# Performance work log

Hardware: AMD Instinct MI355X
Metric: run time of the kernel (lower is better)

The kernel has to match this reference:

```python
import jax, jax.numpy as jnp
import numpy as np

B, C2, H, W = 4, 1024, 64, 64  # features have 2*input_dim channels
CH = C2 // 2                   # 512 = input_dim
HID = CH // 4                  # 128 = hidden_channels


def setup_inputs() -> dict:
    key = jax.random.key(0)
    ks = jax.random.split(key, 6)
    left = jax.random.normal(ks[0], (B, C2, H, W), dtype=jnp.float32)
    right = jax.random.normal(ks[1], (B, C2, H, W), dtype=jnp.float32)
    # 1x1 conv params (weight [out,in], bias [out]) for query/reference projections
    Wq = jax.random.normal(ks[2], (HID, CH), dtype=jnp.float32) * 0.02
    bq = jax.random.normal(ks[3], (HID,), dtype=jnp.float32) * 0.02
    Wk = jax.random.normal(ks[4], (HID, CH), dtype=jnp.float32) * 0.02
    bk = jax.random.normal(ks[5], (HID,), dtype=jnp.float32) * 0.02
    return {"left_features": left, "right_features": right, "Wq": Wq, "bq": bq, "Wk": Wk, "bk": bk}


def _co_attention(qf, rf, Wq, bq, Wk, bk):
    # 1x1 convs == per-pixel channel matmuls
    Q = jnp.einsum('bchw,oc->bohw', qf, Wq) + bq[None, :, None, None]   # [B,HID,H,W]
    K = jnp.einsum('bchw,oc->bohw', rf, Wk) + bk[None, :, None, None]   # [B,HID,H,W]
    b, c, h, w = Q.shape
    Kf = K.reshape(b, c, h * w)                                          # [B,HID,P]
    V = rf.reshape(rf.shape[0], rf.shape[1], h * w)                      # [B,CH,P]
    # attention_map: einsum('bcij,bckl->bijkl') then flatten (kl) == contract channels
    attn = jnp.einsum('bcij,bcp->bijp', Q, Kf)                           # [B,H,W,P]
    attn = jax.nn.softmax(attn, axis=3)
    return jnp.einsum('bijp,bcp->bcij', attn, V)                         # [B,CH,H,W]


def _homo(qf, rf):
    weights = jax.nn.softmax(qf - rf, axis=1)  # softmax over channels
    return rf * weights


def _get_both_differences(q, r, Wq, bq, Wk, bk):
    c = q.shape[1] // 2
    q_orig, q_trans = q[:, :c], q[:, c:]
    r_orig = r[:, :c]
    cross = _co_attention(q_orig, r_orig, Wq, bq, Wk, bk)
    reduce = _homo(q_orig, q_trans)
    return jnp.concatenate([q_orig, cross + reduce], axis=1)


def reference(left_features, right_features, Wq, bq, Wk, bk):
    left_out = _get_both_differences(left_features, right_features, Wq, bq, Wk, bk)
    right_out = _get_both_differences(right_features, left_features, Wq, bq, Wk, bk)
    return (left_out, right_out)
```

## Files before the change

### kernel.cpp

```cpp
#include <hip/hip_runtime.h>
#include <hip/hip_bf16.h>

#define NB 4
#define LOG2E 1.4426950408889634f

typedef unsigned short u16;
typedef __attribute__((ext_vector_type(8))) short bf16x8;
typedef __attribute__((ext_vector_type(4))) float f32x4;

static __device__ __forceinline__ float bf2f(u16 u) {
    union { float f; unsigned v; } x; x.v = ((unsigned)u) << 16; return x.f;
}
static __device__ __forceinline__ u16 f2bf(float f) {
    unsigned v = __builtin_bit_cast(unsigned, f);
    return (u16)((v + 0x7FFFu + ((v >> 16) & 1u)) >> 16);
}
static __device__ __forceinline__ void gload_lds16(const u16* g, u16* l) {
    __builtin_amdgcn_global_load_lds(
        (const __attribute__((address_space(1))) unsigned*)(const void*)g,
        (__attribute__((address_space(3))) unsigned*)(void*)l, 16, 0, 0);
}

__global__ void k_wcvt(const float* __restrict__ Wq, const float* __restrict__ Wk,
                       u16* __restrict__ Wbq, u16* __restrict__ Wbk) {
    int i = blockIdx.x * 1024 + threadIdx.x;
    Wbq[i] = f2bf(Wq[i]);
    Wbk[i] = f2bf(Wk[i]);
}

__global__ void k_cvt(const float* __restrict__ L, const float* __restrict__ R,
                      u16* __restrict__ Lb, u16* __restrict__ Rb, float* __restrict__ out) {
    int i = blockIdx.x * 256 + threadIdx.x;
    int pq = i & 1023;
    int c = (i >> 10) & 511;
    int b = (i >> 19) & 3;
    int side = i >> 21;
    const float* src = (side ? R : L) + ((long)(b * 1024 + c) << 12) + (pq << 2);
    float4 v = *reinterpret_cast<const float4*>(src);
    ushort4 u;
    u.x = f2bf(v.x); u.y = f2bf(v.y); u.z = f2bf(v.z); u.w = f2bf(v.w);
    *reinterpret_cast<ushort4*>((side ? Rb : Lb) + ((long)(b * 512 + c) << 12) + (pq << 2)) = u;
    *reinterpret_cast<float4*>(out + ((long)(side * 4 + b) * 1024 + c) * 4096 + (pq << 2)) = v;
}

__global__ __launch_bounds__(256) void k_proj(
        const u16* __restrict__ Lb, const u16* __restrict__ Rb,
        const u16* __restrict__ Wbq, const u16* __restrict__ Wbk,
        const float* __restrict__ bq, const float* __restrict__ bk,
        u16* __restrict__ QL, u16* __restrict__ KL,
        u16* __restrict__ QR, u16* __restrict__ KR) {
    __shared__ u16 XT[2][64 * 40];
    int pj = blockIdx.x & 15, pt = blockIdx.x >> 4;
    int ty = pj >> 2, b = pj & 3;
    const u16* src; const u16* Wb; const float* bias; u16* dst;
    if (ty == 0)      { src = Lb; Wb = Wbq; bias = bq; dst = QL; }
    else if (ty == 1) { src = Rb; Wb = Wbk; bias = bk; dst = KL; }
    else if (ty == 2) { src = Rb; Wb = Wbq; bias = bq; dst = QR; }
    else              { src = Lb; Wb = Wbk; bias = bk; dst = KR; }
    const u16* X = src + (long)b * 512 * 4096 + pt * 64;
    int tid = threadIdx.x;
    int wv = __builtin_amdgcn_readfirstlane(tid >> 6);
    int lane = tid & 63, g = lane >> 4, li = lane & 15;

    f32x4 acc[8];
#pragma unroll
    for (int ob = 0; ob < 8; ob++)
#pragma unroll
        for (int r = 0; r < 4; r++) acc[ob][r] = bias[ob * 16 + g * 4 + r];

    int c_r = tid >> 3, j = tid & 7;
    bf16x8 gx = *reinterpret_cast<const bf16x8*>(X + (long)c_r * 4096 + j * 8);
#pragma unroll
    for (int k = 0; k < 8; k++) XT[0][(j * 8 + k) * 40 + c_r] = (u16)gx[k];
    __syncthreads();

    for (int cc = 0; cc < 16; cc++) {
        int buf = cc & 1;
        bf16x8 gn;
        if (cc < 15)
            gn = *reinterpret_cast<const bf16x8*>(X + (long)(cc * 32 + 32 + c_r) * 4096 + j * 8);
        bf16x8 xb = *reinterpret_cast<const bf16x8*>(&XT[buf][(wv * 16 + li) * 40 + g * 8]);
#pragma unroll
        for (int ob = 0; ob < 8; ob++) {
            bf16x8 aw = *reinterpret_cast<const bf16x8*>(Wb + (long)(ob * 16 + li) * 512 + cc * 32 + g * 8);
            acc[ob] = __builtin_amdgcn_mfma_f32_16x16x32_bf16(aw, xb, acc[ob], 0, 0, 0);
        }
        if (cc < 15) {
#pragma unroll
            for (int k = 0; k < 8; k++) XT[buf ^ 1][(j * 8 + k) * 40 + c_r] = (u16)gn[k];
        }
        __syncthreads();
    }
    u16* d = dst + ((long)b * 4096 + pt * 64 + wv * 16 + li) * 128;
#pragma unroll
    for (int ob = 0; ob < 8; ob++) {
        uint2 w;
        w.x = (unsigned)f2bf(acc[ob][0]) | ((unsigned)f2bf(acc[ob][1]) << 16);
        w.y = (unsigned)f2bf(acc[ob][2]) | ((unsigned)f2bf(acc[ob][3]) << 16);
        *reinterpret_cast<uint2*>(d + ob * 16 + g * 4) = w;
    }
}

__global__ __launch_bounds__(512, 4) void k_qk(
        const u16* __restrict__ QL, const u16* __restrict__ KL,
        const u16* __restrict__ QR, const u16* __restrict__ KR,
        u16* __restrict__ P, float* __restrict__ sums,
        int bd0, int bdMask, int bdShift) {
    __shared__ u16 Kl[2][8192];
    __shared__ u16 Ps[4096];
    __shared__ float sred[4][2][16];
    int bdl = (int)blockIdx.x & bdMask;
    int rest = (int)blockIdx.x >> bdShift;
    int qtile = rest & 63;
    int ph0 = rest >> 6;
    int bd = bd0 + bdl, dir = bd & 1, b = bd >> 1;
    const u16* Qt = (dir ? QR : QL) + (size_t)b * 4096 * 128;
    const u16* Kt = (dir ? KR : KL) + (size_t)b * 4096 * 128;
    u16* Pbd = P + ((size_t)bdl << 24);
    int q0 = qtile * 64;
    int tid = threadIdx.x;
    int wv = __builtin_amdgcn_readfirstlane(tid >> 6);
    int lane = tid & 63, g = lane >> 4, li = lane & 15;
    int qt = wv >> 1, phw = wv & 1;

#define STAGE_K(BUF, PT)                                                                   \
    {                                                                                      \
        _Pragma("unroll") for (int r0 = 0; r0 < 2; r0++) {                                 \
            int o = r0 * 8192 + tid * 16;                                                  \
            int row = o >> 8, w = o & 255;                                                 \
            int sw = (w ^ ((row & 7) << 4)) >> 1;                                          \
            gload_lds16(Kt + (((size_t)((PT) * 64 + row)) << 7) + sw,                      \
                        &Kl[BUF][r0 * 4096 + wv * 512]);                                   \
        }                                                                                  \
    }

    bf16x8 qf[4];
#pragma unroll
    for (int hc = 0; hc < 4; hc++)
        qf[hc] = *reinterpret_cast<const bf16x8*>(
            Qt + (size_t)(q0 + qt * 16 + li) * 128 + hc * 32 + g * 8);
    float psum = 0.f;
    STAGE_K(0, ph0 * 32)

    for (int tt = 0; tt < 32; tt++) {
        int pt = ph0 * 32 + tt;
        if (tt == 0) asm volatile("s_waitcnt vmcnt(0) lgkmcnt(0)\n\ts_barrier" ::: "memory");
        else         asm volatile("s_waitcnt vmcnt(1) lgkmcnt(0)\n\ts_barrier" ::: "memory");
        if (tt < 31) STAGE_K((tt + 1) & 1, pt + 1)
        int buf = tt & 1;
        f32x4 sv[2];
        sv[0] = (f32x4){0.f, 0.f, 0.f, 0.f};
        sv[1] = (f32x4){0.f, 0.f, 0.f, 0.f};
        __builtin_amdgcn_s_setprio(1);
#pragma unroll
        for (int ps = 0; ps < 2; ps++) {
            int row = phw * 32 + ps * 16 + li;
            unsigned rb = (unsigned)row * 256;
            unsigned sz = (unsigned)((row & 7) << 4);
#pragma unroll
            for (int hc = 0; hc < 4; hc++) {
                bf16x8 kf = *reinterpret_cast<const bf16x8*>(
                    (char*)Kl[buf] + rb + (((unsigned)(hc * 64 + g * 16)) ^ sz));
                sv[ps] = __builtin_amdgcn_mfma_f32_16x16x32_bf16(kf, qf[hc], sv[ps], 0, 0, 0);
            }
        }
        __builtin_amdgcn_s_setprio(0);
        int qrow = qt * 16 + li;
        unsigned qsz = (unsigned)((qrow & 7) << 4);
#pragma unroll
        for (int ps = 0; ps < 2; ps++) {
            float e0 = exp2f(sv[ps][0] * LOG2E);
            float e1 = exp2f(sv[ps][1] * LOG2E);
            float e2 = exp2f(sv[ps][2] * LOG2E);
            float e3 = exp2f(sv[ps][3] * LOG2E);
            psum += (e0 + e1) + (e2 + e3);
            uint2 pk;
            pk.x = (unsigned)f2bf(e0) | ((unsigned)f2bf(e1) << 16);
            pk.y = (unsigned)f2bf(e2) | ((unsigned)f2bf(e3) << 16);
            unsigned off = (unsigned)qrow * 128 +
                           (((unsigned)(phw * 64 + ps * 32 + g * 8)) ^ qsz);
            *reinterpret_cast<uint2*>((char*)Ps + off) = pk;
        }
        asm volatile("s_waitcnt lgkmcnt(0)\n\ts_barrier" ::: "memory");
        {
            uint4 d = *reinterpret_cast<const uint4*>((char*)Ps + tid * 16);
            *reinterpret_cast<uint4*>(
                Pbd + ((size_t)(qtile * 64 + pt) << 12) + tid * 8) = d;
        }
    }
    psum += __shfl_xor(psum, 16);
    psum += __shfl_xor(psum, 32);
    if (lane < 16) sred[qt][phw][li] = psum;
    __syncthreads();
    if (phw == 0 && lane < 16) {
        float s = sred[qt][0][li] + sred[qt][1][li];
        sums[((size_t)ph0 * 8 + bd) * 4096 + q0 + qt * 16 + li] = s;
    }
#undef STAGE_K
}

__global__ __launch_bounds__(256, 2) void k_pv(
        const u16* __restrict__ Lb, const u16* __restrict__ Rb,
        const u16* __restrict__ P, const float* __restrict__ sums,
        float* __restrict__ out, int bd0, int bdMask, int bdShift) {
    __shared__ u16 Tl[2][2][8192];
    int bdl = (int)blockIdx.x & bdMask;
    int idx = (int)blockIdx.x >> bdShift;
    int mtile = idx & 3;
    int ntile = idx >> 2;
    int bd = bd0 + bdl, dir = bd & 1, b = bd >> 1;
    const u16* V = (dir ? Lb : Rb) + (size_t)b * 512 * 4096;
    const u16* Pbd = P + ((size_t)bdl << 24);
    int q0 = ntile * 128, c0 = mtile * 128, qt0 = ntile * 2;
    int tid = threadIdx.x;
    int wv = __builtin_amdgcn_readfirstlane(tid >> 6);
    int lane = tid & 63, g = lane >> 4, li = lane & 15;
    int wr = wv >> 1, wc = wv & 1;

#define STAGE_PV(BUF, T)                                                                   \
    {                                                                                      \
        _Pragma("unroll") for (int r0 = 0; r0 < 4; r0++) {                                 \
            int o = r0 * 4096 + tid * 16;                                                  \
            int row = o >> 7, w = o & 127;                                                 \
            int sw = (w ^ ((row & 7) << 4)) >> 1;                                          \
            gload_lds16(V + (((size_t)(c0 + row)) << 12) + (T) * 64 + sw,                  \
                        &Tl[BUF][0][r0 * 2048 + wv * 512]);                                \
            gload_lds16(Pbd + (((size_t)((qt0 + (r0 >> 1)) * 64 + (T))) << 12) +           \
                            (r0 & 1) * 2048 + tid * 8,                                     \
                        &Tl[BUF][1][r0 * 2048 + wv * 512]);                                \
        }                                                                                  \
    }

    f32x4 acc[4][4];
#pragma unroll
    for (int i = 0; i < 4; i++)
#pragma unroll
        for (int j = 0; j < 4; j++) acc[i][j] = (f32x4){0.f, 0.f, 0.f, 0.f};

    STAGE_PV(0, 0)

    for (int t = 0; t < 64; t++) {
        asm volatile("s_waitcnt vmcnt(0) lgkmcnt(0)\n\ts_barrier" ::: "memory");
        if (t < 63) STAGE_PV((t + 1) & 1, t + 1)
        int buf = t & 1;
        bf16x8 af[4][2], bf[4][2];
#pragma unroll
        for (int mi = 0; mi < 4; mi++) {
            int row = wr * 64 + mi * 16 + li;
            unsigned rb = (unsigned)row * 128, sz = (unsigned)((row & 7) << 4);
#pragma unroll
            for (int kk = 0; kk < 2; kk++)
                af[mi][kk] = *reinterpret_cast<const bf16x8*>(
                    (char*)Tl[buf][0] + rb + (((unsigned)(kk * 64 + g * 16)) ^ sz));
        }
#pragma unroll
        for (int ni = 0; ni < 4; ni++) {
            int row = wc * 64 + ni * 16 + li;
            unsigned rb = (unsigned)row * 128, sz = (unsigned)((row & 7) << 4);
#pragma unroll
            for (int kk = 0; kk < 2; kk++)
                bf[ni][kk] = *reinterpret_cast<const bf16x8*>(
                    (char*)Tl[buf][1] + rb + (((unsigned)(kk * 64 + g * 16)) ^ sz));
        }
        __builtin_amdgcn_s_setprio(1);
#pragma unroll
        for (int kk = 0; kk < 2; kk++)
#pragma unroll
            for (int mi = 0; mi < 4; mi++)
#pragma unroll
                for (int ni = 0; ni < 4; ni++)
                    acc[mi][ni] = __builtin_amdgcn_mfma_f32_16x16x32_bf16(
                        af[mi][kk], bf[ni][kk], acc[mi][ni], 0, 0, 0);
        __builtin_amdgcn_s_setprio(0);
    }

    float* obase = out + ((size_t)(dir * 4 + b) * 1024 + 512) * 4096;
#pragma unroll
    for (int ni = 0; ni < 4; ni++) {
        int q = q0 + wc * 64 + ni * 16 + li;
        float s0 = sums[(size_t)bd * 4096 + q];
        float s1 = sums[((size_t)8 + bd) * 4096 + q];
        float linv = 1.0f / (s0 + s1);
#pragma unroll
        for (int mi = 0; mi < 4; mi++) {
            int c = c0 + wr * 64 + mi * 16 + g * 4;
#pragma unroll
            for (int r = 0; r < 4; r++)
                obase[(size_t)(c + r) * 4096 + q] = acc[mi][ni][r] * linv;
        }
    }
#undef STAGE_PV
}

__global__ __launch_bounds__(256) void k_homo(const float* __restrict__ L,
                                              const float* __restrict__ R,
                                              float* __restrict__ out) {
    __shared__ float4 red[16][16];
    int sb = blockIdx.x & 7, pblk = blockIdx.x >> 3;
    int side = sb & 1, b = sb >> 1;
    const float* src = (side ? R : L) + (long)b * 1024 * 4096;
    float* o = out + (long)(side * 4 + b) * 1024 * 4096;
    int p4 = threadIdx.x & 15, cg = threadIdx.x >> 4;
    int p = pblk * 64 + p4 * 4;
    const float* qo = src + p;
    const float* qt = src + (long)512 * 4096 + p;
    float4 sm = {0.f, 0.f, 0.f, 0.f};
    for (int c = cg * 32; c < cg * 32 + 32; c++) {
        float4 a = *reinterpret_cast<const float4*>(qo + (long)c * 4096);
        float4 t = *reinterpret_cast<const float4*>(qt + (long)c * 4096);
        sm.x += exp2f((a.x - t.x) * LOG2E);
        sm.y += exp2f((a.y - t.y) * LOG2E);
        sm.z += exp2f((a.z - t.z) * LOG2E);
        sm.w += exp2f((a.w - t.w) * LOG2E);
    }
    red[cg][p4] = sm;
    __syncthreads();
    float4 tot = {0.f, 0.f, 0.f, 0.f};
#pragma unroll
    for (int gR = 0; gR < 16; gR++) {
        float4 v = red[gR][p4];
        tot.x += v.x; tot.y += v.y; tot.z += v.z; tot.w += v.w;
    }
    float4 rinv = {1.0f / tot.x, 1.0f / tot.y, 1.0f / tot.z, 1.0f / tot.w};
    for (int c = cg * 32; c < cg * 32 + 32; c++) {
        float4 a = *reinterpret_cast<const float4*>(qo + (long)c * 4096);
        float4 t = *reinterpret_cast<const float4*>(qt + (long)c * 4096);
        float4* op = reinterpret_cast<float4*>(o + (long)(512 + c) * 4096 + p);
        float4 cur = *op;
        cur.x += t.x * exp2f((a.x - t.x) * LOG2E) * rinv.x;
        cur.y += t.y * exp2f((a.y - t.y) * LOG2E) * rinv.y;
        cur.z += t.z * exp2f((a.z - t.z) * LOG2E) * rinv.z;
        cur.w += t.w * exp2f((a.w - t.w) * LOG2E) * rinv.w;
        *op = cur;
    }
}

extern "C" void kernel_launch(void* const* d_in, const int* in_sizes, int n_in,
                              void* d_out, int out_size, void* d_ws, size_t ws_size,
                              hipStream_t stream) {
    const float* L  = (const float*)d_in[0];
    const float* R  = (const float*)d_in[1];
    const float* Wq = (const float*)d_in[2];
    const float* bq = (const float*)d_in[3];
    const float* Wk = (const float*)d_in[4];
    const float* bk = (const float*)d_in[5];
    float* out = (float*)d_out;
    char* ws = (char*)d_ws;

    size_t off = 0;
    u16* Wbq = (u16*)(ws + off); off += (size_t)128 * 512 * 2;
    u16* Wbk = (u16*)(ws + off); off += (size_t)128 * 512 * 2;
    u16* QL = (u16*)(ws + off); off += (size_t)NB * 4096 * 128 * 2;
    u16* KL = (u16*)(ws + off); off += (size_t)NB * 4096 * 128 * 2;
    u16* QR = (u16*)(ws + off); off += (size_t)NB * 4096 * 128 * 2;
    u16* KR = (u16*)(ws + off); off += (size_t)NB * 4096 * 128 * 2;
    u16* Lb = (u16*)(ws + off); off += (size_t)NB * 512 * 4096 * 2;
    u16* Rb = (u16*)(ws + off); off += (size_t)NB * 512 * 4096 * 2;
    float* sums = (float*)(ws + off); off += (size_t)2 * 8 * 4096 * 4;
    off = (off + 255) & ~(size_t)255;
    u16* Pb = (u16*)(ws + off);

    size_t pchunk4 = (size_t)4 * 4096 * 4096 * 2;
    int nbd, bdShift;
    if (ws_size >= off + pchunk4) { nbd = 4; bdShift = 2; }
    else                          { nbd = 1; bdShift = 0; }
    int bdMask = nbd - 1;
    int nchunk = 8 / nbd;

    k_wcvt <<<64,    1024, 0, stream>>>(Wq, Wk, Wbq, Wbk);
    k_cvt  <<<16384, 256,  0, stream>>>(L, R, Lb, Rb, out);
    k_proj <<<1024,  256,  0, stream>>>(Lb, Rb, Wbq, Wbk, bq, bk, QL, KL, QR, KR);
    for (int c = 0; c < nchunk; c++) {
        k_qk <<<nbd * 128, 512, 0, stream>>>(QL, KL, QR, KR, Pb, sums,
                                             c * nbd, bdMask, bdShift);
        k_pv <<<nbd * 128, 256, 0, stream>>>(Lb, Rb, Pb, sums, out,
                                             c * nbd, bdMask, bdShift);
    }
    k_homo <<<512,   256,  0, stream>>>(L, R, out);
}
```

Baseline: 418.5 us.

## Fuse homo softmax into conversion pass and add it in PV epilogue

Adds a k_cvtf kernel that, while converting the originals to bf16 and copying them to the output, also computes the channel-softmax numerators t*exp(a-t) as bf16 and per-pixel partial sums. The PV kernel epilogue then adds the normalized homo term before its single output store. This removes the separate k_homo pass, which re-read both full float inputs and read-modify-wrote the output. In exchange it needs extra workspace, adds a bf16 rounding to the homo term, and stores unnormalized exp values that could lose range for large differences.

```diff
diff --git a/kernel.cpp b/kernel.cpp
--- a/kernel.cpp
+++ b/kernel.cpp
@@ -26,6 +26,59 @@
     int i = blockIdx.x * 1024 + threadIdx.x;
     Wbq[i] = f2bf(Wq[i]);
     Wbk[i] = f2bf(Wk[i]);
+}
+
+__global__ __launch_bounds__(256) void k_cvtf(
+        const float* __restrict__ L, const float* __restrict__ R,
+        u16* __restrict__ Lb, u16* __restrict__ Rb,
+        u16* __restrict__ web, float* __restrict__ sumsH, float* __restrict__ out) {
+    __shared__ float4 red[16][16];
+    int idx = blockIdx.x;
+    int sb = idx & 7, pblk = (idx >> 3) & 63, cpart = idx >> 9;
+    int side = sb & 1, b = sb >> 1;
+    int osb = side * 4 + b;
+    const float* src = (side ? R : L) + (size_t)b * 1024 * 4096;
+    int tid = threadIdx.x;
+    int p4 = tid & 15, cg = tid >> 4;
+    int p = pblk * 64 + p4 * 4;
+    int cbase = cpart * 128 + cg * 8;
+    const float* ao = src + (size_t)cbase * 4096 + p;
+    const float* at = src + (size_t)(512 + cbase) * 4096 + p;
+    u16* lbdst = (side ? Rb : Lb) + ((size_t)b * 512 + cbase) * 4096 + p;
+    float* odst = out + ((size_t)osb * 1024 + cbase) * 4096 + p;
+    u16* wdst = web + ((size_t)osb * 512 + cbase) * 4096 + p;
+    float4 sm = {0.f, 0.f, 0.f, 0.f};
+#pragma unroll
+    for (int cc = 0; cc < 8; cc++) {
+        float4 a = *reinterpret_cast<const float4*>(ao + (size_t)cc * 4096);
+        float4 t = *reinterpret_cast<const float4*>(at + (size_t)cc * 4096);
+        ushort4 ub;
+        ub.x = f2bf(a.x); ub.y = f2bf(a.y); ub.z = f2bf(a.z); ub.w = f2bf(a.w);
+        *reinterpret_cast<ushort4*>(lbdst + (size_t)cc * 4096) = ub;
+        *reinterpret_cast<float4*>(odst + (size_t)cc * 4096) = a;
+        float4 e;
+        e.x = exp2f((a.x - t.x) * LOG2E);
+        e.y = exp2f((a.y - t.y) * LOG2E);
+        e.z = exp2f((a.z - t.z) * LOG2E);
+        e.w = exp2f((a.w - t.w) * LOG2E);
+        sm.x += e.x; sm.y += e.y; sm.z += e.z; sm.w += e.w;
+        ushort4 wb_;
+        wb_.x = f2bf(t.x * e.x); wb_.y = f2bf(t.y * e.y);
+        wb_.z = f2bf(t.z * e.z); wb_.w = f2bf(t.w * e.w);
+        *reinterpret_cast<ushort4*>(wdst + (size_t)cc * 4096) = wb_;
+    }
+    red[cg][p4] = sm;
+    __syncthreads();
+    if (tid < 16) {
+        float4 tot = {0.f, 0.f, 0.f, 0.f};
+#pragma unroll
+        for (int gR = 0; gR < 16; gR++) {
+            float4 v = red[gR][tid];
+            tot.x += v.x; tot.y += v.y; tot.z += v.z; tot.w += v.w;
+        }
+        *reinterpret_cast<float4*>(
+            sumsH + ((size_t)cpart * 8 + osb) * 4096 + pblk * 64 + tid * 4) = tot;
+    }
 }
 
 __global__ void k_cvt(const float* __restrict__ L, const float* __restrict__ R,
@@ -199,9 +252,11 @@
 #undef STAGE_K
 }
 
+template<int FUSEH>
 __global__ __launch_bounds__(256, 2) void k_pv(
         const u16* __restrict__ Lb, const u16* __restrict__ Rb,
         const u16* __restrict__ P, const float* __restrict__ sums,
+        const u16* __restrict__ web, const float* __restrict__ sumsH,
         float* __restrict__ out, int bd0, int bdMask, int bdShift) {
     __shared__ u16 Tl[2][2][8192];
     int bdl = (int)blockIdx.x & bdMask;
@@ -209,6 +264,7 @@
     int mtile = idx & 3;
     int ntile = idx >> 2;
     int bd = bd0 + bdl, dir = bd & 1, b = bd >> 1;
+    int osb = dir * 4 + b;
     const u16* V = (dir ? Lb : Rb) + (size_t)b * 512 * 4096;
     const u16* Pbd = P + ((size_t)bdl << 24);
     int q0 = ntile * 128, c0 = mtile * 128, qt0 = ntile * 2;
@@ -274,19 +330,31 @@
         __builtin_amdgcn_s_setprio(0);
     }
 
-    float* obase = out + ((size_t)(dir * 4 + b) * 1024 + 512) * 4096;
+    float* obase = out + ((size_t)osb * 1024 + 512) * 4096;
+    const u16* wb = web + (size_t)osb * 512 * 4096;
 #pragma unroll
     for (int ni = 0; ni < 4; ni++) {
         int q = q0 + wc * 64 + ni * 16 + li;
         float s0 = sums[(size_t)bd * 4096 + q];
         float s1 = sums[((size_t)8 + bd) * 4096 + q];
         float linv = 1.0f / (s0 + s1);
+        float hinv = 0.f;
+        if (FUSEH) {
+            float hs = sumsH[(size_t)osb * 4096 + q] +
+                       sumsH[((size_t)8 + osb) * 4096 + q] +
+                       sumsH[((size_t)16 + osb) * 4096 + q] +
+                       sumsH[((size_t)24 + osb) * 4096 + q];
+            hinv = 1.0f / hs;
+        }
 #pragma unroll
         for (int mi = 0; mi < 4; mi++) {
             int c = c0 + wr * 64 + mi * 16 + g * 4;
 #pragma unroll
-            for (int r = 0; r < 4; r++)
-                obase[(size_t)(c + r) * 4096 + q] = acc[mi][ni][r] * linv;
+            for (int r = 0; r < 4; r++) {
+                float v = acc[mi][ni][r] * linv;
+                if (FUSEH) v += bf2f(wb[(size_t)(c + r) * 4096 + q]) * hinv;
+                obase[(size_t)(c + r) * 4096 + q] = v;
+            }
         }
     }
 #undef STAGE_PV
@@ -357,24 +425,38 @@
     u16* Lb = (u16*)(ws + off); off += (size_t)NB * 512 * 4096 * 2;
     u16* Rb = (u16*)(ws + off); off += (size_t)NB * 512 * 4096 * 2;
     float* sums = (float*)(ws + off); off += (size_t)2 * 8 * 4096 * 4;
+    float* sumsH = (float*)(ws + off); off += (size_t)4 * 8 * 4096 * 4;
+    size_t off_nofuse = off;
+    u16* web = (u16*)(ws + off); off += (size_t)8 * 512 * 4096 * 2;
     off = (off + 255) & ~(size_t)255;
-    u16* Pb = (u16*)(ws + off);
-
     size_t pchunk4 = (size_t)4 * 4096 * 4096 * 2;
-    int nbd, bdShift;
-    if (ws_size >= off + pchunk4) { nbd = 4; bdShift = 2; }
-    else                          { nbd = 1; bdShift = 0; }
-    int bdMask = nbd - 1;
-    int nchunk = 8 / nbd;
-
-    k_wcvt <<<64,    1024, 0, stream>>>(Wq, Wk, Wbq, Wbk);
-    k_cvt  <<<16384, 256,  0, stream>>>(L, R, Lb, Rb, out);
-    k_proj <<<1024,  256,  0, stream>>>(Lb, Rb, Wbq, Wbk, bq, bk, QL, KL, QR, KR);
-    for (int c = 0; c < nchunk; c++) {
-        k_qk <<<nbd * 128, 512, 0, stream>>>(QL, KL, QR, KR, Pb, sums,
-                                             c * nbd, bdMask, bdShift);
-        k_pv <<<nbd * 128, 256, 0, stream>>>(Lb, Rb, Pb, sums, out,
-                                             c * nbd, bdMask, bdShift);
-    }
-    k_homo <<<512,   256,  0, stream>>>(L, R, out);
-}
+    size_t pchunk1 = (size_t)4096 * 4096 * 2;
+
+    k_wcvt <<<64, 1024, 0, stream>>>(Wq, Wk, Wbq, Wbk);
+
+    if (ws_size >= off + pchunk4) {
+        u16* Pb = (u16*)(ws + off);
+        k_cvtf <<<2048, 256, 0, stream>>>(L, R, Lb, Rb, web, sumsH, out);
+        k_proj <<<1024, 256, 0, stream>>>(Lb, Rb, Wbq, Wbk, bq, bk, QL, KL, QR, KR);
+        for (int c = 0; c < 2; c++) {
+            k_qk    <<<512, 512, 0, stream>>>(QL, KL, QR, KR, Pb, sums, c * 4, 3, 2);
+            k_pv<1> <<<512, 256, 0, stream>>>(Lb, Rb, Pb, sums, web, sumsH, out, c * 4, 3, 2);
+        }
+    } else {
+        int nbd, bdShift;
+        size_t poff = (off_nofuse + 255) & ~(size_t)255;
+        if (ws_size >= poff + pchunk4) { nbd = 4; bdShift = 2; }
+        else                           { nbd = 1; bdShift = 0; }
+        int bdMask = nbd - 1, nchunk = 8 / nbd;
+        u16* Pb = (u16*)(ws + poff);
+        k_cvt  <<<16384, 256, 0, stream>>>(L, R, Lb, Rb, out);
+        k_proj <<<1024,  256, 0, stream>>>(Lb, Rb, Wbq, Wbk, bq, bk, QL, KL, QR, KR);
+        for (int c = 0; c < nchunk; c++) {
+            k_qk    <<<nbd * 128, 512, 0, stream>>>(QL, KL, QR, KR, Pb, sums,
+                                                    c * nbd, bdMask, bdShift);
+            k_pv<0> <<<nbd * 128, 256, 0, stream>>>(Lb, Rb, Pb, sums, web, sumsH, out,
+                                                    c * nbd, bdMask, bdShift);
+        }
+        k_homo <<<512, 256, 0, stream>>>(L, R, out);
+    }
+}
```

Measured after the change: 404.6 us. 3.3% less time.
